# Optimization experiments

Measured on AMD Instinct MI355X. Metric: run time of the kernel, lower is better.

## Reference

```python
import jax, jax.numpy as jnp
import numpy as np

B, S, F, DK = 4, 2048, 1024, 1024

def setup_inputs() -> dict:
    key = jax.random.key(0)
    ks = jax.random.split(key, 9)
    sF = 1.0 / np.sqrt(F)
    sD = 1.0 / np.sqrt(DK)
    return {
        "x":  jax.random.normal(ks[0], (B, S, F), dtype=jnp.float32),
        "Wq": jax.random.normal(ks[1], (DK, F), dtype=jnp.float32) * sF,
        "bq": jax.random.normal(ks[2], (DK,), dtype=jnp.float32) * sF,
        "Wk": jax.random.normal(ks[3], (DK, F), dtype=jnp.float32) * sF,
        "bk": jax.random.normal(ks[4], (DK,), dtype=jnp.float32) * sF,
        "Wv": jax.random.normal(ks[5], (DK, F), dtype=jnp.float32) * sF,
        "bv": jax.random.normal(ks[6], (DK,), dtype=jnp.float32) * sF,
        "Wo": jax.random.normal(ks[7], (F, DK), dtype=jnp.float32) * sD,
        "bo": jax.random.normal(ks[8], (F,), dtype=jnp.float32) * sD,
    }

def reference(x, Wq, bq, Wk, bk, Wv, bv, Wo, bo):
    # Linear layers (torch convention: y = x @ W.T + b)
    q = jnp.einsum('bsf,df->bsd', x, Wq) + bq  # (B,S,DK)
    k = jnp.einsum('bsf,df->bsd', x, Wk) + bk  # (B,S,DK)
    v = jnp.einsum('bsf,df->bsd', x, Wv) + bv  # (B,S,DK)
    scale = 1.0 / (q.shape[-1] ** 0.5)
    scores = jnp.einsum('bqd,bkd->bqk', q, k) * scale  # (B,Sq,Sk)
    # Faithful to original: softmax over dim=-2 (the QUERY axis)
    attn = jax.nn.softmax(scores, axis=-2)
    ctx = jnp.einsum('bqk,bkd->bqd', attn, v)  # (B,S,DK)
    out = jnp.einsum('bsd,fd->bsf', ctx, Wo) + bo  # (B,S,F)
    return out
```

## Files before the change

### kernel.cpp

```cpp
#include <hip/hip_runtime.h>
#include <hip/hip_bf16.h>
#include <math.h>

typedef __bf16 bf16_t;
typedef __bf16 bf16x8 __attribute__((ext_vector_type(8)));
typedef float f32x4 __attribute__((ext_vector_type(4)));


__device__ __forceinline__ void g2l16(const bf16_t* g, bf16_t* l) {
  __builtin_amdgcn_global_load_lds(
      (const __attribute__((address_space(1))) void*)g,
      (__attribute__((address_space(3))) void*)l, 16, 0, 0);
}

__device__ __forceinline__ void xcdswz(int& bx, int& by, int& bz) {
  const int gx = gridDim.x, gy = gridDim.y;
  const int n = gx * gy * gridDim.z;
  int f = bx + gx * (by + gy * bz);
  const int cpx = n >> 3;
  int s = (f & 7) * cpx + (f >> 3);
  bx = s % gx; s /= gx; by = s % gy; bz = s / gy;
}

__device__ __forceinline__ bf16x8 rdf(const char* base, int row, int kbyte) {
  int off = (row << 7) + kbyte;
  off ^= (row & 7) << 4;
  return *reinterpret_cast<const bf16x8*>(base + off);
}


__global__ __launch_bounds__(256) void cast_f32_to_bf16(
    const float* __restrict__ in, bf16_t* __restrict__ out, long n) {
  long i = ((long)blockIdx.x * 256 + threadIdx.x) * 8;
  if (i >= n) return;
  float4 a = *reinterpret_cast<const float4*>(in + i);
  float4 b = *reinterpret_cast<const float4*>(in + i + 4);
  bf16x8 o;
  o[0] = (bf16_t)a.x; o[1] = (bf16_t)a.y; o[2] = (bf16_t)a.z; o[3] = (bf16_t)a.w;
  o[4] = (bf16_t)b.x; o[5] = (bf16_t)b.y; o[6] = (bf16_t)b.z; o[7] = (bf16_t)b.w;
  *reinterpret_cast<bf16x8*>(out + i) = o;
}

__global__ __launch_bounds__(256) void cast_w4(
    const float* __restrict__ w0, const float* __restrict__ w1,
    const float* __restrict__ w2, const float* __restrict__ w3,
    bf16_t* __restrict__ o0, bf16_t* __restrict__ o1,
    bf16_t* __restrict__ o2, bf16_t* __restrict__ o3) {
  const int sel = blockIdx.x >> 9;
  const int blk = blockIdx.x & 511;
  const float* in = sel == 0 ? w0 : (sel == 1 ? w1 : (sel == 2 ? w2 : w3));
  bf16_t* out = sel == 0 ? o0 : (sel == 1 ? o1 : (sel == 2 ? o2 : o3));
  long i = ((long)blk * 256 + threadIdx.x) * 8;
  float4 a = *reinterpret_cast<const float4*>(in + i);
  float4 b = *reinterpret_cast<const float4*>(in + i + 4);
  bf16x8 o;
  o[0] = (bf16_t)a.x; o[1] = (bf16_t)a.y; o[2] = (bf16_t)a.z; o[3] = (bf16_t)a.w;
  o[4] = (bf16_t)b.x; o[5] = (bf16_t)b.y; o[6] = (bf16_t)b.z; o[7] = (bf16_t)b.w;
  *reinterpret_cast<bf16x8*>(out + i) = o;
}


#define STAGE256(d, o, h, t) do {                                              \
  const bf16_t* gsrc_ = ((o) ? Bb : Ab) + (long)((h) * 128 + srl) * K +        \
                        (long)(t) * 64 + sgsw;                                 \
  bf16_t* ldsb_ = &lds[d][o][(h) * 8192] + ldst;                               \
  g2l16(gsrc_, ldsb_);                                                         \
  g2l16(gsrc_ + 64L * K, ldsb_ + 4096);                                        \
} while (0)

#define AREAD256(d, qm) do {                                                   \
  const char* Ab_ = (const char*)&lds[d][0][0];                                \
  int r_ = (qm) * 128 + wr2 * 64 + rA;                                         \
  a0 = rdf(Ab_, r_, kb);      a1 = rdf(Ab_, r_, kb + 64);                      \
  a2 = rdf(Ab_, r_ + 16, kb); a3 = rdf(Ab_, r_ + 16, kb + 64);                 \
  a4 = rdf(Ab_, r_ + 32, kb); a5 = rdf(Ab_, r_ + 32, kb + 64);                 \
  a6 = rdf(Ab_, r_ + 48, kb); a7 = rdf(Ab_, r_ + 48, kb + 64);                 \
} while (0)

#define BREAD256(d, qn, r0v, r1v, r2v, r3v) do {                               \
  const char* Bb_ = (const char*)&lds[d][1][0];                                \
  int c_ = (qn) * 128 + wc2 * 32 + rA;                                         \
  r0v = rdf(Bb_, c_, kb);      r1v = rdf(Bb_, c_, kb + 64);                    \
  r2v = rdf(Bb_, c_ + 16, kb); r3v = rdf(Bb_, c_ + 16, kb + 64);               \
} while (0)

#define MFMA16(qm, qn, b0v, b1v, b2v, b3v) do {                                \
  acc[(qm)*4+0][(qn)*2+0] = __builtin_amdgcn_mfma_f32_16x16x32_bf16(a0, b0v, acc[(qm)*4+0][(qn)*2+0], 0,0,0); \
  acc[(qm)*4+0][(qn)*2+0] = __builtin_amdgcn_mfma_f32_16x16x32_bf16(a1, b1v, acc[(qm)*4+0][(qn)*2+0], 0,0,0); \
  acc[(qm)*4+1][(qn)*2+0] = __builtin_amdgcn_mfma_f32_16x16x32_bf16(a2, b0v, acc[(qm)*4+1][(qn)*2+0], 0,0,0); \
  acc[(qm)*4+1][(qn)*2+0] = __builtin_amdgcn_mfma_f32_16x16x32_bf16(a3, b1v, acc[(qm)*4+1][(qn)*2+0], 0,0,0); \
  acc[(qm)*4+2][(qn)*2+0] = __builtin_amdgcn_mfma_f32_16x16x32_bf16(a4, b0v, acc[(qm)*4+2][(qn)*2+0], 0,0,0); \
  acc[(qm)*4+2][(qn)*2+0] = __builtin_amdgcn_mfma_f32_16x16x32_bf16(a5, b1v, acc[(qm)*4+2][(qn)*2+0], 0,0,0); \
  acc[(qm)*4+3][(qn)*2+0] = __builtin_amdgcn_mfma_f32_16x16x32_bf16(a6, b0v, acc[(qm)*4+3][(qn)*2+0], 0,0,0); \
  acc[(qm)*4+3][(qn)*2+0] = __builtin_amdgcn_mfma_f32_16x16x32_bf16(a7, b1v, acc[(qm)*4+3][(qn)*2+0], 0,0,0); \
  acc[(qm)*4+0][(qn)*2+1] = __builtin_amdgcn_mfma_f32_16x16x32_bf16(a0, b2v, acc[(qm)*4+0][(qn)*2+1], 0,0,0); \
  acc[(qm)*4+0][(qn)*2+1] = __builtin_amdgcn_mfma_f32_16x16x32_bf16(a1, b3v, acc[(qm)*4+0][(qn)*2+1], 0,0,0); \
  acc[(qm)*4+1][(qn)*2+1] = __builtin_amdgcn_mfma_f32_16x16x32_bf16(a2, b2v, acc[(qm)*4+1][(qn)*2+1], 0,0,0); \
  acc[(qm)*4+1][(qn)*2+1] = __builtin_amdgcn_mfma_f32_16x16x32_bf16(a3, b3v, acc[(qm)*4+1][(qn)*2+1], 0,0,0); \
  acc[(qm)*4+2][(qn)*2+1] = __builtin_amdgcn_mfma_f32_16x16x32_bf16(a4, b2v, acc[(qm)*4+2][(qn)*2+1], 0,0,0); \
  acc[(qm)*4+2][(qn)*2+1] = __builtin_amdgcn_mfma_f32_16x16x32_bf16(a5, b3v, acc[(qm)*4+2][(qn)*2+1], 0,0,0); \
  acc[(qm)*4+3][(qn)*2+1] = __builtin_amdgcn_mfma_f32_16x16x32_bf16(a6, b2v, acc[(qm)*4+3][(qn)*2+1], 0,0,0); \
  acc[(qm)*4+3][(qn)*2+1] = __builtin_amdgcn_mfma_f32_16x16x32_bf16(a7, b3v, acc[(qm)*4+3][(qn)*2+1], 0,0,0); \
} while (0)

#define VMC(n) asm volatile("s_waitcnt vmcnt(" #n ")" ::: "memory")

#define PH_ENTER() do {                                                        \
  __builtin_amdgcn_s_barrier();                                                \
  asm volatile("s_waitcnt lgkmcnt(0)" ::: "memory");                           \
  __builtin_amdgcn_s_setprio(1);                                               \
} while (0)

#define PH_EXIT() do {                                                         \
  __builtin_amdgcn_s_setprio(0);                                               \
  __builtin_amdgcn_s_barrier();                                                \
} while (0)

template <int EPI>
__launch_bounds__(512, 2)
__global__ void gemm256(const bf16_t* __restrict__ A, const bf16_t* __restrict__ B,
                        int K, float alpha,
                        void* __restrict__ C0, void* __restrict__ C1, void* __restrict__ C2,
                        const float* __restrict__ bias0, const float* __restrict__ bias1,
                        const float* __restrict__ bias2,
                        int Ncols, long sA, long sB, long sC) {
  __shared__ bf16_t lds[2][2][16384];

  int bx = blockIdx.x, by = blockIdx.y, bz = blockIdx.z;
  xcdswz(bx, by, bz);

  const int tid = threadIdx.x;
  const int lane = tid & 63;
  const int w = tid >> 6;
  const int wr2 = w >> 2;
  const int wc2 = w & 3;
  const int rA = lane & 15;
  const int kb = (lane >> 4) << 4;

  const int bm = bx * 256;
  const int bn = by * 256;
  const bf16_t* Ab = A + (long)bz * sA + (long)bm * K;
  const bf16_t* Bb = B + (long)bz * sB + (long)bn * K;

  const int srl = tid >> 3;
  const int sgr = tid & 7;
  const int sgsw = (sgr ^ (srl & 7)) * 8;
  const int ldst = srl * 64 + sgr * 8;

  f32x4 acc[8][4] = {};
  bf16x8 a0, a1, a2, a3, a4, a5, a6, a7;
  bf16x8 p0, p1, p2, p3, q0, q1, q2, q3;

  const int NT = K >> 6;

  STAGE256(0, 0, 0, 0);
  STAGE256(0, 1, 0, 0);
  STAGE256(0, 1, 1, 0);
  STAGE256(0, 0, 1, 0);
  STAGE256(1, 0, 0, 1);
  STAGE256(1, 1, 0, 1);
  STAGE256(1, 1, 1, 1);
  STAGE256(1, 0, 1, 1);
  VMC(12);
  __builtin_amdgcn_s_barrier();

  int t = 0;
  for (int it = 0; it < NT / 2 - 1; ++it, t += 2) {
    AREAD256(0, 0); BREAD256(0, 0, p0, p1, p2, p3);
    VMC(10);
    PH_ENTER(); MFMA16(0, 0, p0, p1, p2, p3); PH_EXIT();
    BREAD256(0, 1, q0, q1, q2, q3);
    STAGE256(0, 0, 0, t + 2); STAGE256(0, 1, 0, t + 2);
    VMC(12);
    PH_ENTER(); MFMA16(0, 1, q0, q1, q2, q3); PH_EXIT();
    AREAD256(0, 1);
    STAGE256(0, 1, 1, t + 2);
    PH_ENTER(); MFMA16(1, 0, p0, p1, p2, p3); PH_EXIT();
    STAGE256(0, 0, 1, t + 2);
    VMC(12);
    PH_ENTER(); MFMA16(1, 1, q0, q1, q2, q3); PH_EXIT();
    AREAD256(1, 0); BREAD256(1, 0, p0, p1, p2, p3);
    VMC(10);
    PH_ENTER(); MFMA16(0, 0, p0, p1, p2, p3); PH_EXIT();
    BREAD256(1, 1, q0, q1, q2, q3);
    STAGE256(1, 0, 0, t + 3); STAGE256(1, 1, 0, t + 3);
    VMC(12);
    PH_ENTER(); MFMA16(0, 1, q0, q1, q2, q3); PH_EXIT();
    AREAD256(1, 1);
    STAGE256(1, 1, 1, t + 3);
    PH_ENTER(); MFMA16(1, 0, p0, p1, p2, p3); PH_EXIT();
    STAGE256(1, 0, 1, t + 3);
    VMC(12);
    PH_ENTER(); MFMA16(1, 1, q0, q1, q2, q3); PH_EXIT();
  }

  AREAD256(0, 0); BREAD256(0, 0, p0, p1, p2, p3);
  VMC(10);
  PH_ENTER(); MFMA16(0, 0, p0, p1, p2, p3); PH_EXIT();
  BREAD256(0, 1, q0, q1, q2, q3);
  VMC(8);
  PH_ENTER(); MFMA16(0, 1, q0, q1, q2, q3); PH_EXIT();
  AREAD256(0, 1);
  PH_ENTER(); MFMA16(1, 0, p0, p1, p2, p3); PH_EXIT();
  VMC(4);
  PH_ENTER(); MFMA16(1, 1, q0, q1, q2, q3); PH_EXIT();
  AREAD256(1, 0); BREAD256(1, 0, p0, p1, p2, p3);
  VMC(2);
  PH_ENTER(); MFMA16(0, 0, p0, p1, p2, p3); PH_EXIT();
  BREAD256(1, 1, q0, q1, q2, q3);
  VMC(0);
  PH_ENTER(); MFMA16(0, 1, q0, q1, q2, q3); PH_EXIT();
  AREAD256(1, 1);
  PH_ENTER(); MFMA16(1, 0, p0, p1, p2, p3); PH_EXIT();
  PH_ENTER(); MFMA16(1, 1, q0, q1, q2, q3); PH_EXIT();

  const int rr = (lane >> 4) * 4;
  const int cc = lane & 15;
#pragma unroll
  for (int qm = 0; qm < 2; ++qm)
#pragma unroll
    for (int m = 0; m < 4; ++m) {
      const int grow = bm + qm * 128 + wr2 * 64 + m * 16 + rr;
#pragma unroll
      for (int qn = 0; qn < 2; ++qn)
#pragma unroll
        for (int n = 0; n < 2; ++n) {
          const int gcol = bn + qn * 128 + wc2 * 32 + n * 16 + cc;
          const f32x4 v = acc[qm * 4 + m][qn * 2 + n];
          if (EPI == 1) {
            const int sel = gcol >> 10;
            const int lcol = gcol & 1023;
            const float* bp = sel == 0 ? bias0 : (sel == 1 ? bias1 : bias2);
            bf16_t* op = sel == 0 ? (bf16_t*)C0 : (sel == 1 ? (bf16_t*)C1 : (bf16_t*)C2);
            const float bv = bp[lcol];
#pragma unroll
            for (int j = 0; j < 4; ++j)
              op[(long)(grow + j) * 1024 + lcol] = (bf16_t)(v[j] + bv);
          } else {
            float* C = (float*)C0;
            const float bv = bias0[gcol];
#pragma unroll
            for (int j = 0; j < 4; ++j)
              C[(long)(grow + j) * Ncols + gcol] = v[j] + bv;
          }
        }
    }
  (void)Ncols; (void)sC;
}


template <int OUT_BF16, int HAS_BIAS, int EXPO>
__launch_bounds__(256, 2)
__global__ void gemm_bt(const bf16_t* __restrict__ A, const bf16_t* __restrict__ B,
                        const float* __restrict__ bias, void* __restrict__ Cv,
                        int M, int N, int K, float alpha,
                        long sA, long sB, long sC) {
  int bxi = blockIdx.x, byi = blockIdx.y, bzi = blockIdx.z;
  xcdswz(bxi, byi, bzi);
  const bf16_t* Ab = A + (long)bzi * sA;
  const bf16_t* Bb = B + (long)bzi * sB;
  const int bm = bxi * 128;
  const int bn = byi * 128;

  __shared__ bf16_t sAt[128 * 32];
  __shared__ bf16_t sBt[128 * 32];

  const int tid = threadIdx.x;
  const int lane = tid & 63;
  const int w = tid >> 6;
  const int wr = (w >> 1) * 64;
  const int wc = (w & 1) * 64;

  f32x4 acc[4][4] = {};

  const int r0 = tid >> 2;
  const int c0 = (tid & 3) * 8;
  const int r1 = 64 + (tid >> 2);
  const long lds0 = (long)tid * 8;
  const long lds1 = 2048 + (long)tid * 8;

  const int arow = wr + (lane & 15);
  const int brow = wc + (lane & 15);
  const int koff = (lane >> 4) * 8;

  const int nK = K >> 5;
  for (int kt = 0; kt < nK; ++kt) {
    const int k0 = kt << 5;
    g2l16(Ab + (long)(bm + r0) * K + k0 + c0, sAt + lds0);
    g2l16(Ab + (long)(bm + r1) * K + k0 + c0, sAt + lds1);
    g2l16(Bb + (long)(bn + r0) * K + k0 + c0, sBt + lds0);
    g2l16(Bb + (long)(bn + r1) * K + k0 + c0, sBt + lds1);
    __syncthreads();

    bf16x8 af[4], bfr[4];
#pragma unroll
    for (int m = 0; m < 4; ++m)
      af[m] = *reinterpret_cast<const bf16x8*>(sAt + (arow + m * 16) * 32 + koff);
#pragma unroll
    for (int n = 0; n < 4; ++n)
      bfr[n] = *reinterpret_cast<const bf16x8*>(sBt + (brow + n * 16) * 32 + koff);
#pragma unroll
    for (int m = 0; m < 4; ++m)
#pragma unroll
      for (int n = 0; n < 4; ++n)
        acc[m][n] = __builtin_amdgcn_mfma_f32_16x16x32_bf16(af[m], bfr[n], acc[m][n], 0, 0, 0);
    __syncthreads();
  }

  const int rbase = bm + wr + (lane >> 4) * 4;
  const int cbase = bn + wc + (lane & 15);
#pragma unroll
  for (int n = 0; n < 4; ++n) {
    const int col = cbase + n * 16;
    float bv = 0.f;
    if (HAS_BIAS) bv = bias[col];
#pragma unroll
    for (int m = 0; m < 4; ++m) {
      const int row0 = rbase + m * 16;
#pragma unroll
      for (int j = 0; j < 4; ++j) {
        float v = acc[m][n][j] * alpha + bv;
        if (EXPO) {
          bf16_t* C = (bf16_t*)Cv + (long)bzi * sC;
          C[(long)(row0 + j) * N + col] = (bf16_t)__expf(v);
        } else if (OUT_BF16) {
          bf16_t* C = (bf16_t*)Cv + (long)bzi * sC;
          C[(long)(row0 + j) * N + col] = (bf16_t)v;
        } else {
          float* C = (float*)Cv + (long)bzi * sC;
          C[(long)(row0 + j) * N + col] = v;
        }
      }
    }
  }
}


__global__ __launch_bounds__(256) void col_partial(const bf16_t* __restrict__ P,
                                                   float* __restrict__ part) {
  const int kc = blockIdx.x, qc = blockIdx.y, b = blockIdx.z;
  const int t = threadIdx.x;
  const int tk = t & 31;
  const int tq = t >> 5;
  const bf16_t* base = P + ((long)b * 2048 + (long)qc * 256 + tq) * 2048 + kc * 256 + tk * 8;
  float s[8] = {};
  for (int q = 0; q < 256; q += 8) {
    bf16x8 v = *reinterpret_cast<const bf16x8*>(base + (long)q * 2048);
#pragma unroll
    for (int u = 0; u < 8; ++u) s[u] += (float)v[u];
  }
  __shared__ float red[8][256];
#pragma unroll
  for (int u = 0; u < 8; ++u) red[tq][tk * 8 + u] = s[u];
  __syncthreads();
  float tot = 0.f;
#pragma unroll
  for (int r = 0; r < 8; ++r) tot += red[r][t];
  part[((long)b * 8 + qc) * 2048 + kc * 256 + t] = tot;
}


__global__ __launch_bounds__(256) void vscale_T(const bf16_t* __restrict__ V,
                                                const float* __restrict__ part,
                                                bf16_t* __restrict__ VsT) {
  const int b = blockIdx.z;
  const int r0 = blockIdx.x * 64;
  const int c0 = blockIdx.y * 64;
  __shared__ bf16_t tile[64][72];
  const int t = threadIdx.x;
  const int i = t >> 2;
  const int cj = (t & 3) * 16;
  const int k = r0 + i;
  float rs = 0.f;
#pragma unroll
  for (int r = 0; r < 8; ++r) rs += part[((long)b * 8 + r) * 2048 + k];
  const float ri = 1.0f / rs;
  const bf16_t* src = V + ((long)b * 2048 + k) * 1024 + c0 + cj;
  bf16x8 a0 = *reinterpret_cast<const bf16x8*>(src);
  bf16x8 a1 = *reinterpret_cast<const bf16x8*>(src + 8);
#pragma unroll
  for (int u = 0; u < 8; ++u) {
    tile[i][cj + u] = (bf16_t)((float)a0[u] * ri);
    tile[i][cj + 8 + u] = (bf16_t)((float)a1[u] * ri);
  }
  __syncthreads();
  const int j = t >> 2;
  const int rc = (t & 3) * 16;
  bf16x8 o0, o1;
#pragma unroll
  for (int u = 0; u < 8; ++u) o0[u] = tile[rc + u][j];
#pragma unroll
  for (int u = 0; u < 8; ++u) o1[u] = tile[rc + 8 + u][j];
  bf16_t* dst = VsT + ((long)b * 1024 + c0 + j) * 2048 + r0 + rc;
  *reinterpret_cast<bf16x8*>(dst) = o0;
  *reinterpret_cast<bf16x8*>(dst + 8) = o1;
}


extern "C" void kernel_launch(void* const* d_in, const int* in_sizes, int n_in,
                              void* d_out, int out_size, void* d_ws, size_t ws_size,
                              hipStream_t stream) {
  const float* x  = (const float*)d_in[0];
  const float* Wq = (const float*)d_in[1];
  const float* bq = (const float*)d_in[2];
  const float* Wk = (const float*)d_in[3];
  const float* bk = (const float*)d_in[4];
  const float* Wv = (const float*)d_in[5];
  const float* bv = (const float*)d_in[6];
  const float* Wo = (const float*)d_in[7];
  const float* bo = (const float*)d_in[8];
  float* out = (float*)d_out;
  char* ws = (char*)d_ws;

  const long MB = 1024L * 1024L;
  bf16_t* xb    = (bf16_t*)(ws + 0);
  bf16_t* Wqkvb = (bf16_t*)(ws + 16 * MB);
  bf16_t* Wob   = (bf16_t*)(ws + 22 * MB);
  bf16_t* Qb    = (bf16_t*)(ws + 24 * MB);
  bf16_t* Kb    = (bf16_t*)(ws + 40 * MB);
  bf16_t* Vb    = (bf16_t*)(ws + 56 * MB);
  bf16_t* Pp    = (bf16_t*)(ws + 72 * MB);
  float*  part  = (float*)(ws + 168 * MB);
  bf16_t* VsT   = (bf16_t*)(ws + 0);
  bf16_t* ctxb  = (bf16_t*)(ws + 24 * MB);

  cast_f32_to_bf16<<<4096, 256, 0, stream>>>(x, xb, 8388608);
  cast_w4<<<2048, 256, 0, stream>>>(Wq, Wk, Wv, Wo,
                                    Wqkvb, Wqkvb + 1048576, Wqkvb + 2097152, Wob);

  gemm256<1><<<dim3(32, 12, 1), 512, 0, stream>>>(
      xb, Wqkvb, 1024, 1.0f, Qb, Kb, Vb, bq, bk, bv, 3072, 0, 0, 0);

  gemm_bt<1, 0, 1><<<dim3(16, 16, 4), 256, 0, stream>>>(
      Qb, Kb, nullptr, Pp, 2048, 2048, 1024, 0.03125f,
      2048L * 1024, 2048L * 1024, 2048L * 2048);

  col_partial<<<dim3(8, 8, 4), 256, 0, stream>>>(Pp, part);

  vscale_T<<<dim3(32, 16, 4), 256, 0, stream>>>(Vb, part, VsT);

  dim3 gctx(16, 8, 4);
  gemm_bt<1, 0, 0><<<gctx, 256, 0, stream>>>(Pp, VsT, nullptr, ctxb, 2048, 1024, 2048, 1.0f,
                                             2048L * 2048, 1024L * 2048, 2048L * 1024);

  gemm256<3><<<dim3(32, 4, 1), 512, 0, stream>>>(
      ctxb, Wob, 1024, 1.0f, out, nullptr, nullptr, bo, nullptr, nullptr,
      1024, 0, 0, 0);

  (void)in_sizes; (void)n_in; (void)out_size; (void)ws_size;
}
```

Measured before the change: 303.4 us.

## Fuse softmax column sums into score GEMM epilogue via atomics

The exp-score GEMM epilogue now accumulates per-column sums of the exponentials, reduces them across lanes with shuffles, and adds them into a per-batch column-sum buffer with atomicAdd. This removes the separate col_partial pass that re-read the 32 MB bf16 score matrix. The two cast kernels are merged into one prep launch that also zeroes the sum buffer. The cost is atomic contention and sums taken from fp32 values rather than the rounded bf16 ones.

```diff
diff --git a/kernel.cpp b/kernel.cpp
--- a/kernel.cpp
+++ b/kernel.cpp
@@ -29,34 +29,40 @@
 }
 
 
-__global__ __launch_bounds__(256) void cast_f32_to_bf16(
-    const float* __restrict__ in, bf16_t* __restrict__ out, long n) {
-  long i = ((long)blockIdx.x * 256 + threadIdx.x) * 8;
-  if (i >= n) return;
-  float4 a = *reinterpret_cast<const float4*>(in + i);
-  float4 b = *reinterpret_cast<const float4*>(in + i + 4);
-  bf16x8 o;
-  o[0] = (bf16_t)a.x; o[1] = (bf16_t)a.y; o[2] = (bf16_t)a.z; o[3] = (bf16_t)a.w;
-  o[4] = (bf16_t)b.x; o[5] = (bf16_t)b.y; o[6] = (bf16_t)b.z; o[7] = (bf16_t)b.w;
-  *reinterpret_cast<bf16x8*>(out + i) = o;
-}
-
-__global__ __launch_bounds__(256) void cast_w4(
-    const float* __restrict__ w0, const float* __restrict__ w1,
-    const float* __restrict__ w2, const float* __restrict__ w3,
-    bf16_t* __restrict__ o0, bf16_t* __restrict__ o1,
-    bf16_t* __restrict__ o2, bf16_t* __restrict__ o3) {
-  const int sel = blockIdx.x >> 9;
-  const int blk = blockIdx.x & 511;
-  const float* in = sel == 0 ? w0 : (sel == 1 ? w1 : (sel == 2 ? w2 : w3));
-  bf16_t* out = sel == 0 ? o0 : (sel == 1 ? o1 : (sel == 2 ? o2 : o3));
-  long i = ((long)blk * 256 + threadIdx.x) * 8;
-  float4 a = *reinterpret_cast<const float4*>(in + i);
-  float4 b = *reinterpret_cast<const float4*>(in + i + 4);
-  bf16x8 o;
-  o[0] = (bf16_t)a.x; o[1] = (bf16_t)a.y; o[2] = (bf16_t)a.z; o[3] = (bf16_t)a.w;
-  o[4] = (bf16_t)b.x; o[5] = (bf16_t)b.y; o[6] = (bf16_t)b.z; o[7] = (bf16_t)b.w;
-  *reinterpret_cast<bf16x8*>(out + i) = o;
+__global__ __launch_bounds__(256) void prep(
+    const float* __restrict__ x, const float* __restrict__ w0,
+    const float* __restrict__ w1, const float* __restrict__ w2,
+    const float* __restrict__ w3,
+    bf16_t* __restrict__ xb, bf16_t* __restrict__ o0, bf16_t* __restrict__ o1,
+    bf16_t* __restrict__ o2, bf16_t* __restrict__ o3,
+    float* __restrict__ part) {
+  const int bx = blockIdx.x;
+  const int t = threadIdx.x;
+  if (bx < 4096) {
+    long i = ((long)bx * 256 + t) * 8;
+    float4 a = *reinterpret_cast<const float4*>(x + i);
+    float4 b = *reinterpret_cast<const float4*>(x + i + 4);
+    bf16x8 o;
+    o[0] = (bf16_t)a.x; o[1] = (bf16_t)a.y; o[2] = (bf16_t)a.z; o[3] = (bf16_t)a.w;
+    o[4] = (bf16_t)b.x; o[5] = (bf16_t)b.y; o[6] = (bf16_t)b.z; o[7] = (bf16_t)b.w;
+    *reinterpret_cast<bf16x8*>(xb + i) = o;
+  } else if (bx < 6144) {
+    const int sel = (bx - 4096) >> 9;
+    const int blk = (bx - 4096) & 511;
+    const float* in = sel == 0 ? w0 : (sel == 1 ? w1 : (sel == 2 ? w2 : w3));
+    bf16_t* out = sel == 0 ? o0 : (sel == 1 ? o1 : (sel == 2 ? o2 : o3));
+    long i = ((long)blk * 256 + t) * 8;
+    float4 a = *reinterpret_cast<const float4*>(in + i);
+    float4 b = *reinterpret_cast<const float4*>(in + i + 4);
+    bf16x8 o;
+    o[0] = (bf16_t)a.x; o[1] = (bf16_t)a.y; o[2] = (bf16_t)a.z; o[3] = (bf16_t)a.w;
+    o[4] = (bf16_t)b.x; o[5] = (bf16_t)b.y; o[6] = (bf16_t)b.z; o[7] = (bf16_t)b.w;
+    *reinterpret_cast<bf16x8*>(out + i) = o;
+  } else {
+    long i = ((long)(bx - 6144) * 256 + t) * 4;
+    float4 z = {0.f, 0.f, 0.f, 0.f};
+    *reinterpret_cast<float4*>(part + i) = z;
+  }
 }
 
 
@@ -253,6 +259,7 @@
 __launch_bounds__(256, 2)
 __global__ void gemm_bt(const bf16_t* __restrict__ A, const bf16_t* __restrict__ B,
                         const float* __restrict__ bias, void* __restrict__ Cv,
+                        float* __restrict__ part,
                         int M, int N, int K, float alpha,
                         long sA, long sB, long sC) {
   int bxi = blockIdx.x, byi = blockIdx.y, bzi = blockIdx.z;
@@ -314,6 +321,7 @@
     const int col = cbase + n * 16;
     float bv = 0.f;
     if (HAS_BIAS) bv = bias[col];
+    float cs = 0.f;
 #pragma unroll
     for (int m = 0; m < 4; ++m) {
       const int row0 = rbase + m * 16;
@@ -322,7 +330,9 @@
         float v = acc[m][n][j] * alpha + bv;
         if (EXPO) {
           bf16_t* C = (bf16_t*)Cv + (long)bzi * sC;
-          C[(long)(row0 + j) * N + col] = (bf16_t)__expf(v);
+          float e = __expf(v);
+          C[(long)(row0 + j) * N + col] = (bf16_t)e;
+          cs += e;
         } else if (OUT_BF16) {
           bf16_t* C = (bf16_t*)Cv + (long)bzi * sC;
           C[(long)(row0 + j) * N + col] = (bf16_t)v;
@@ -332,31 +342,12 @@
         }
       }
     }
+    if (EXPO) {
+      cs += __shfl_down(cs, 32);
+      cs += __shfl_down(cs, 16);
+      if (lane < 16) atomicAdd(&part[(long)bzi * 2048 + col], cs);
+    }
   }
-}
-
-
-__global__ __launch_bounds__(256) void col_partial(const bf16_t* __restrict__ P,
-                                                   float* __restrict__ part) {
-  const int kc = blockIdx.x, qc = blockIdx.y, b = blockIdx.z;
-  const int t = threadIdx.x;
-  const int tk = t & 31;
-  const int tq = t >> 5;
-  const bf16_t* base = P + ((long)b * 2048 + (long)qc * 256 + tq) * 2048 + kc * 256 + tk * 8;
-  float s[8] = {};
-  for (int q = 0; q < 256; q += 8) {
-    bf16x8 v = *reinterpret_cast<const bf16x8*>(base + (long)q * 2048);
-#pragma unroll
-    for (int u = 0; u < 8; ++u) s[u] += (float)v[u];
-  }
-  __shared__ float red[8][256];
-#pragma unroll
-  for (int u = 0; u < 8; ++u) red[tq][tk * 8 + u] = s[u];
-  __syncthreads();
-  float tot = 0.f;
-#pragma unroll
-  for (int r = 0; r < 8; ++r) tot += red[r][t];
-  part[((long)b * 8 + qc) * 2048 + kc * 256 + t] = tot;
 }
 
 
@@ -371,10 +362,7 @@
   const int i = t >> 2;
   const int cj = (t & 3) * 16;
   const int k = r0 + i;
-  float rs = 0.f;
-#pragma unroll
-  for (int r = 0; r < 8; ++r) rs += part[((long)b * 8 + r) * 2048 + k];
-  const float ri = 1.0f / rs;
+  const float ri = 1.0f / part[(long)b * 2048 + k];
   const bf16_t* src = V + ((long)b * 2048 + k) * 1024 + c0 + cj;
   bf16x8 a0 = *reinterpret_cast<const bf16x8*>(src);
   bf16x8 a1 = *reinterpret_cast<const bf16x8*>(src + 8);
@@ -424,23 +412,22 @@
   bf16_t* VsT   = (bf16_t*)(ws + 0);
   bf16_t* ctxb  = (bf16_t*)(ws + 24 * MB);
 
-  cast_f32_to_bf16<<<4096, 256, 0, stream>>>(x, xb, 8388608);
-  cast_w4<<<2048, 256, 0, stream>>>(Wq, Wk, Wv, Wo,
-                                    Wqkvb, Wqkvb + 1048576, Wqkvb + 2097152, Wob);
+  prep<<<6152, 256, 0, stream>>>(x, Wq, Wk, Wv, Wo,
+                                 xb, Wqkvb, Wqkvb + 1048576, Wqkvb + 2097152, Wob,
+                                 part);
 
   gemm256<1><<<dim3(32, 12, 1), 512, 0, stream>>>(
       xb, Wqkvb, 1024, 1.0f, Qb, Kb, Vb, bq, bk, bv, 3072, 0, 0, 0);
 
   gemm_bt<1, 0, 1><<<dim3(16, 16, 4), 256, 0, stream>>>(
-      Qb, Kb, nullptr, Pp, 2048, 2048, 1024, 0.03125f,
+      Qb, Kb, nullptr, Pp, part, 2048, 2048, 1024, 0.03125f,
       2048L * 1024, 2048L * 1024, 2048L * 2048);
 
-  col_partial<<<dim3(8, 8, 4), 256, 0, stream>>>(Pp, part);
-
   vscale_T<<<dim3(32, 16, 4), 256, 0, stream>>>(Vb, part, VsT);
 
   dim3 gctx(16, 8, 4);
-  gemm_bt<1, 0, 0><<<gctx, 256, 0, stream>>>(Pp, VsT, nullptr, ctxb, 2048, 1024, 2048, 1.0f,
+  gemm_bt<1, 0, 0><<<gctx, 256, 0, stream>>>(Pp, VsT, nullptr, ctxb, nullptr,
+                                             2048, 1024, 2048, 1.0f,
                                              2048L * 2048, 1024L * 2048, 2048L * 1024);
 
   gemm256<3><<<dim3(32, 4, 1), 512, 0, stream>>>(
```

Measured after the change: 295.7 us. 1.03x faster.
